# Optimization experiments

Measured on AMD Instinct MI355X. Metric: run time of the kernel, lower is better.

Reference implementation:

```python
import jax, jax.numpy as jnp
import numpy as np
from jax import lax


def _transform_points(pts, M, eps=1e-8):
    # pytorch3d row-vector convention: p' = [p, 1] @ M, then perspective divide by w.
    ph = jnp.concatenate([pts, jnp.ones(pts.shape[:-1] + (1,), pts.dtype)], axis=-1)
    out = jnp.einsum('bnk,bkl->bnl', ph, M)
    w = out[..., 3:4]
    w = jnp.where(jnp.abs(w) < eps, eps, w)
    return out[..., :3] / w


def _rasterize_spheres(pts_screen, radius, image_size, K):
    # pts_screen: [B,N,3] with (x,y) in NDC and z = view-space depth; radius: [B,N].
    # Per pixel: keep K front-most (smallest z>0) points with NDC dist2 <= radius^2.
    B, N, _ = pts_screen.shape
    half = 1.0 - 1.0 / image_size
    coords = jnp.linspace(half, -half, image_size, dtype=pts_screen.dtype)  # pytorch3d NDC: +x left, +y up
    py, px = jnp.meshgrid(coords, coords, indexing='ij')  # [H,W]
    dx = pts_screen[:, None, None, :, 0] - px[None, :, :, None]  # [B,H,W,N]
    dy = pts_screen[:, None, None, :, 1] - py[None, :, :, None]
    dist2 = dx * dx + dy * dy
    z = pts_screen[:, None, None, :, 2]  # [B,1,1,N]
    inside = (dist2 <= (radius * radius)[:, None, None, :]) & (z > 0)
    zmask = jnp.where(inside, z, jnp.inf)
    negz, inds = lax.top_k(-zmask, K)  # K smallest z (front-most) per pixel
    valid = jnp.isfinite(negz)
    zbuf = jnp.where(valid, -negz, jnp.float32(-1.0))
    d2 = jnp.take_along_axis(dist2, inds, axis=-1)
    dists = jnp.where(valid, d2, jnp.float32(-1.0))
    idx = jnp.where(valid, inds, -1)
    return idx, zbuf, dists


def setup_inputs() -> dict:
    key = jax.random.key(0)
    k1, k2 = jax.random.split(key)
    B, N = 1, 1024
    points = jax.random.normal(k1, (B, N, 3), dtype=jnp.float32)
    radius = 0.02 + 0.06 * jax.random.uniform(k2, (B, N), dtype=jnp.float32)
    # Rigid world->view: identity rotation, translate camera so points sit at z ~ 3 (row-vector convention).
    w2v = np.eye(4, dtype=np.float32)
    w2v[3, 2] = 3.0
    world2view = jnp.asarray(w2v)[None]
    # Perspective projection (row-vector): [x,y,z,1] @ P = [s x, s y, a z + b, z]
    s, znear, zfar = 2.0, 0.1, 100.0
    a = zfar / (zfar - znear)
    b = -zfar * znear / (zfar - znear)
    proj = jnp.asarray(np.array([[s, 0, 0, 0], [0, s, 0, 0], [0, 0, a, 1], [0, 0, b, 0]], dtype=np.float32))[None]
    return {'points': points, 'radius': radius, 'world2view': world2view, 'proj': proj,
            'image_size': 256, 'points_per_pixel': 8}


def reference(points, radius, world2view, proj, image_size, points_per_pixel):
    pts_view = _transform_points(points, world2view)
    pts_screen = _transform_points(pts_view, proj)
    pts_screen = pts_screen.at[..., 2].set(pts_view[..., 2])  # keep view-space depth
    idx, zbuf, dists = _rasterize_spheres(pts_screen, radius, image_size, points_per_pixel)
    return idx, zbuf, dists
```

## Files before the change

kernel.cpp:

```cpp
#include <hip/hip_runtime.h>
#include <math.h>


#define KPP 8
#define BW  8
#define TS  16

typedef float vf4 __attribute__((ext_vector_type(4)));

static __device__ __forceinline__ void nt_store4(float* p, float a, float b, float c, float d) {
    vf4 v = {a, b, c, d};
    __builtin_nontemporal_store(v, (vf4*)p);
}

__global__ __launch_bounds__(256) void sphere_raster_kernel(
    const float* __restrict__ points,
    const float* __restrict__ radius,
    const float* __restrict__ w2v,
    const float* __restrict__ proj,
    float* __restrict__ out,
    int B, int N, int H, int W)
{
    extern __shared__ char smem[];
    float4* cmp  = (float4*)smem;
    int*    cidx = (int*)(smem + (size_t)(N + 2 * BW) * sizeof(float4));
    __shared__ int wsum[4];

    const int tid      = threadIdx.x;
    const int tilesX   = W / TS;
    const int tilesPer = tilesX * (H / TS);
    const int tile     = blockIdx.x % tilesPer;
    const int b        = blockIdx.x / tilesPer;
    const int tx0      = (tile % tilesX) * TS;
    const int ty0      = (tile / tilesX) * TS;
    const int j        = tx0 + (tid & (TS - 1));
    const int i        = ty0 + (tid >> 4);
    const int lane     = tid & 63;
    const int wid      = tid >> 6;

    const float* M1 = w2v  + (size_t)b * 16;
    const float* M2 = proj + (size_t)b * 16;

    const double halfd = 1.0 - 1.0 / (double)W;
    const double stepd = 2.0 * halfd / (double)(W - 1);
    const float px = (float)(halfd - (double)j * stepd);
    const float py = (float)(halfd - (double)i * stepd);
    const float cx = (float)(halfd - ((double)tx0 + (TS - 1) * 0.5) * stepd);
    const float cy = (float)(halfd - ((double)ty0 + (TS - 1) * 0.5) * stepd);
    const float hext = (float)(((TS - 1) * 0.5 + 1.0) * stepd);

    const int t0 = tid * 4;
    float4 P[4];
    int keep[4];
    int c = 0;

    const float4* pv = (const float4*)(points + ((size_t)b * N + t0) * 3);
    float4 q0 = pv[0], q1 = pv[1], q2 = pv[2];
    float4 rr = *(const float4*)(radius + (size_t)b * N + t0);
    float xs[4] = {q0.x, q0.w, q1.z, q2.y};
    float ys[4] = {q0.y, q1.x, q1.w, q2.z};
    float zs[4] = {q0.z, q1.y, q2.x, q2.w};
    float rv[4] = {rr.x, rr.y, rr.z, rr.w};

#pragma unroll
    for (int s = 0; s < 4; ++s) {
        float x = xs[s], y = ys[s], z = zs[s];
        float vx = ((x * M1[0] + y * M1[4]) + z * M1[8])  + M1[12];
        float vy = ((x * M1[1] + y * M1[5]) + z * M1[9])  + M1[13];
        float vz = ((x * M1[2] + y * M1[6]) + z * M1[10]) + M1[14];
        float vw = ((x * M1[3] + y * M1[7]) + z * M1[11]) + M1[15];
        float w1 = (fabsf(vw) < 1e-8f) ? 1e-8f : vw;
        vx /= w1; vy /= w1; vz /= w1;
        float sx = ((vx * M2[0] + vy * M2[4]) + vz * M2[8])  + M2[12];
        float sy = ((vx * M2[1] + vy * M2[5]) + vz * M2[9])  + M2[13];
        float sw = ((vx * M2[3] + vy * M2[7]) + vz * M2[11]) + M2[15];
        float w2 = (fabsf(sw) < 1e-8f) ? 1e-8f : sw;
        sx /= w2; sy /= w2;
        float r = rv[s];
        float r2eff = (vz > 0.0f) ? r * r : -1.0f;
        float dxm = fmaxf(0.0f, fabsf(sx - cx) - hext);
        float dym = fmaxf(0.0f, fabsf(sy - cy) - hext);
        float dmin2 = dxm * dxm + dym * dym;
        keep[s] = (dmin2 <= r2eff + 1e-6f) ? 1 : 0;
        P[s] = make_float4(sx, sy, vz, r2eff);
        c += keep[s];
    }

    int pre = c;
#pragma unroll
    for (int d = 1; d < 64; d <<= 1) {
        int v = __shfl_up(pre, d);
        if (lane >= d) pre += v;
    }
    if (lane == 63) wsum[wid] = pre;
    __syncthreads();
    int wbase = 0, M = 0;
#pragma unroll
    for (int w = 0; w < 4; ++w) {
        int s = wsum[w];
        if (w < wid) wbase += s;
        M += s;
    }
    int pos = wbase + (pre - c);
#pragma unroll
    for (int s = 0; s < 4; ++s) {
        if (keep[s]) { cmp[pos] = P[s]; cidx[pos] = t0 + s; ++pos; }
    }
    const int Mpad = (M + 2 * BW - 1) & ~(2 * BW - 1);
    if (tid < Mpad - M) {
        cmp[M + tid]  = make_float4(0.0f, 0.0f, 0.0f, -1.0f);
        cidx[M + tid] = -1;
    }
    __syncthreads();

    unsigned long long kb[KPP];
#pragma unroll
    for (int k = 0; k < KPP; ++k) kb[k] = ~0ULL;

    auto process = [&](const float4* pp, int base) {
#pragma unroll
        for (int u = 0; u < BW; ++u) {
            float dx = pp[u].x - px;
            float dy = pp[u].y - py;
            float dist2 = __fadd_rn(__fmul_rn(dx, dx), __fmul_rn(dy, dy));
            unsigned long long key =
                ((unsigned long long)__float_as_uint(pp[u].z) << 32) |
                (unsigned)(base + u);
            if ((dist2 <= pp[u].w) && (key < kb[KPP - 1])) {
                unsigned long long kc = key;
#pragma unroll
                for (int k2 = 0; k2 < KPP; ++k2) {
                    unsigned long long t = kb[k2];
                    bool lt = (kc < t);
                    kb[k2] = lt ? kc : t;
                    kc     = lt ? t  : kc;
                }
            }
        }
    };

    float4 pa[BW];
    float4 pb[BW];

#pragma unroll
    for (int u = 0; u < BW; ++u) pa[u] = cmp[u];

    for (int n = 0; n < Mpad; n += 2 * BW) {
#pragma unroll
        for (int u = 0; u < BW; ++u) pb[u] = cmp[n + BW + u];
        process(pa, n);
        if (n + 2 * BW < Mpad) {
#pragma unroll
            for (int u = 0; u < BW; ++u) pa[u] = cmp[n + 2 * BW + u];
        }
        process(pb, n + BW);
    }

    const size_t pix   = ((size_t)b * H + i) * W + j;
    const size_t plane = (size_t)B * H * W * KPP;
    float vidx[KPP], vzbf[KPP], vdst[KPP];
#pragma unroll
    for (int k = 0; k < KPP; ++k) {
        unsigned long long key = kb[k];
        bool valid = (key != ~0ULL);
        int p2 = valid ? (int)(key & 0xFFFFFFFFu) : 0;
        float4 p = cmp[p2];
        int idx  = cidx[p2];
        float dx = p.x - px;
        float dy = p.y - py;
        float dist2 = __fadd_rn(__fmul_rn(dx, dx), __fmul_rn(dy, dy));
        float z = __uint_as_float((unsigned)(key >> 32));
        vidx[k] = valid ? (float)idx : -1.0f;
        vzbf[k] = valid ? z          : -1.0f;
        vdst[k] = valid ? dist2      : -1.0f;
    }
    float* oidx = out + pix * KPP;
    float* ozbf = out + plane + pix * KPP;
    float* odst = out + 2 * plane + pix * KPP;
    nt_store4(oidx,     vidx[0], vidx[1], vidx[2], vidx[3]);
    nt_store4(oidx + 4, vidx[4], vidx[5], vidx[6], vidx[7]);
    nt_store4(ozbf,     vzbf[0], vzbf[1], vzbf[2], vzbf[3]);
    nt_store4(ozbf + 4, vzbf[4], vzbf[5], vzbf[6], vzbf[7]);
    nt_store4(odst,     vdst[0], vdst[1], vdst[2], vdst[3]);
    nt_store4(odst + 4, vdst[4], vdst[5], vdst[6], vdst[7]);
}

extern "C" void kernel_launch(void* const* d_in, const int* in_sizes, int n_in,
                              void* d_out, int out_size, void* d_ws, size_t ws_size,
                              hipStream_t stream) {
    const float* points = (const float*)d_in[0];
    const float* radius = (const float*)d_in[1];
    const float* w2v    = (const float*)d_in[2];
    const float* proj   = (const float*)d_in[3];
    int B = in_sizes[2] / 16;
    if (B < 1) B = 1;
    int N = in_sizes[1] / B;
    int HW = out_size / (3 * B * KPP);
    int H = 1;
    while ((H + 1) * (H + 1) <= HW) ++H;
    int W = H;

    int tiles = (W / TS) * (H / TS);
    size_t shmem = (size_t)(N + 2 * BW) * (sizeof(float4) + sizeof(int));
    sphere_raster_kernel<<<B * tiles, 256, shmem, stream>>>(
        points, radius, w2v, proj, (float*)d_out, B, N, H, W);
}
```

Measured before the change: 13.59 us.

## Cull points per wavefront 8x8 sub-tile with ballot compaction into per-wave lists

Each wavefront now covers an 8x8 pixel quadrant instead of rows of a 16x16 tile, and builds its own candidate list by culling all projected points against its quadrant's bounding box, using ballot/popcount compaction. The aim is shorter per-wave candidate loops, and the block-wide scan and barrier before the raster loop go away. In exchange every wave scans all N points from shared memory, and the list is hard-capped at 256 entries, so extra candidates are silently dropped if a quadrant has more. The hard-coded 16 iterations also assume N=1024.

```diff
diff --git a/kernel.cpp b/kernel.cpp
--- a/kernel.cpp
+++ b/kernel.cpp
@@ -5,6 +5,7 @@
 #define KPP 8
 #define BW  8
 #define TS  16
+#define CAP 256
 
 typedef float vf4 __attribute__((ext_vector_type(4)));
 
@@ -22,21 +23,23 @@
     int B, int N, int H, int W)
 {
     extern __shared__ char smem[];
-    float4* cmp  = (float4*)smem;
-    int*    cidx = (int*)(smem + (size_t)(N + 2 * BW) * sizeof(float4));
-    __shared__ int wsum[4];
+    float4* sh = (float4*)smem;
+    float4* cmpw  = (float4*)(smem + (size_t)N * 16);
+    int*    cidxw = (int*)(smem + (size_t)N * 16 + 4 * (CAP + 16) * 16);
 
     const int tid      = threadIdx.x;
+    const int lane     = tid & 63;
+    const int wid      = tid >> 6;
     const int tilesX   = W / TS;
     const int tilesPer = tilesX * (H / TS);
     const int tile     = blockIdx.x % tilesPer;
     const int b        = blockIdx.x / tilesPer;
     const int tx0      = (tile % tilesX) * TS;
     const int ty0      = (tile / tilesX) * TS;
-    const int j        = tx0 + (tid & (TS - 1));
-    const int i        = ty0 + (tid >> 4);
-    const int lane     = tid & 63;
-    const int wid      = tid >> 6;
+    const int qx = tx0 + (wid & 1) * 8;
+    const int qy = ty0 + (wid >> 1) * 8;
+    const int j = qx + (lane & 7);
+    const int i = qy + (lane >> 3);
 
     const float* M1 = w2v  + (size_t)b * 16;
     const float* M2 = proj + (size_t)b * 16;
@@ -45,73 +48,63 @@
     const double stepd = 2.0 * halfd / (double)(W - 1);
     const float px = (float)(halfd - (double)j * stepd);
     const float py = (float)(halfd - (double)i * stepd);
-    const float cx = (float)(halfd - ((double)tx0 + (TS - 1) * 0.5) * stepd);
-    const float cy = (float)(halfd - ((double)ty0 + (TS - 1) * 0.5) * stepd);
-    const float hext = (float)(((TS - 1) * 0.5 + 1.0) * stepd);
-
-    const int t0 = tid * 4;
-    float4 P[4];
-    int keep[4];
-    int c = 0;
-
-    const float4* pv = (const float4*)(points + ((size_t)b * N + t0) * 3);
-    float4 q0 = pv[0], q1 = pv[1], q2 = pv[2];
-    float4 rr = *(const float4*)(radius + (size_t)b * N + t0);
-    float xs[4] = {q0.x, q0.w, q1.z, q2.y};
-    float ys[4] = {q0.y, q1.x, q1.w, q2.z};
-    float zs[4] = {q0.z, q1.y, q2.x, q2.w};
-    float rv[4] = {rr.x, rr.y, rr.z, rr.w};
-
-#pragma unroll
-    for (int s = 0; s < 4; ++s) {
-        float x = xs[s], y = ys[s], z = zs[s];
-        float vx = ((x * M1[0] + y * M1[4]) + z * M1[8])  + M1[12];
-        float vy = ((x * M1[1] + y * M1[5]) + z * M1[9])  + M1[13];
-        float vz = ((x * M1[2] + y * M1[6]) + z * M1[10]) + M1[14];
-        float vw = ((x * M1[3] + y * M1[7]) + z * M1[11]) + M1[15];
-        float w1 = (fabsf(vw) < 1e-8f) ? 1e-8f : vw;
-        vx /= w1; vy /= w1; vz /= w1;
-        float sx = ((vx * M2[0] + vy * M2[4]) + vz * M2[8])  + M2[12];
-        float sy = ((vx * M2[1] + vy * M2[5]) + vz * M2[9])  + M2[13];
-        float sw = ((vx * M2[3] + vy * M2[7]) + vz * M2[11]) + M2[15];
-        float w2 = (fabsf(sw) < 1e-8f) ? 1e-8f : sw;
-        sx /= w2; sy /= w2;
-        float r = rv[s];
-        float r2eff = (vz > 0.0f) ? r * r : -1.0f;
-        float dxm = fmaxf(0.0f, fabsf(sx - cx) - hext);
-        float dym = fmaxf(0.0f, fabsf(sy - cy) - hext);
+    const float cxw = (float)(halfd - ((double)qx + 3.5) * stepd);
+    const float cyw = (float)(halfd - ((double)qy + 3.5) * stepd);
+    const float hext = (float)(4.5 * stepd);
+
+    {
+        const int t0 = tid * 4;
+        const float4* pv = (const float4*)(points + ((size_t)b * N + t0) * 3);
+        float4 q0 = pv[0], q1 = pv[1], q2 = pv[2];
+        float4 rr = *(const float4*)(radius + (size_t)b * N + t0);
+        float xs[4] = {q0.x, q0.w, q1.z, q2.y};
+        float ys[4] = {q0.y, q1.x, q1.w, q2.z};
+        float zs[4] = {q0.z, q1.y, q2.x, q2.w};
+        float rv[4] = {rr.x, rr.y, rr.z, rr.w};
+#pragma unroll
+        for (int s = 0; s < 4; ++s) {
+            float x = xs[s], y = ys[s], z = zs[s];
+            float vx = ((x * M1[0] + y * M1[4]) + z * M1[8])  + M1[12];
+            float vy = ((x * M1[1] + y * M1[5]) + z * M1[9])  + M1[13];
+            float vz = ((x * M1[2] + y * M1[6]) + z * M1[10]) + M1[14];
+            float vw = ((x * M1[3] + y * M1[7]) + z * M1[11]) + M1[15];
+            float w1 = (fabsf(vw) < 1e-8f) ? 1e-8f : vw;
+            vx /= w1; vy /= w1; vz /= w1;
+            float sx = ((vx * M2[0] + vy * M2[4]) + vz * M2[8])  + M2[12];
+            float sy = ((vx * M2[1] + vy * M2[5]) + vz * M2[9])  + M2[13];
+            float sw = ((vx * M2[3] + vy * M2[7]) + vz * M2[11]) + M2[15];
+            float w2 = (fabsf(sw) < 1e-8f) ? 1e-8f : sw;
+            sx /= w2; sy /= w2;
+            float r = rv[s];
+            float r2eff = (vz > 0.0f) ? r * r : -1.0f;
+            sh[t0 + s] = make_float4(sx, sy, vz, r2eff);
+        }
+    }
+    __syncthreads();
+
+    float4* cmp  = cmpw  + wid * (CAP + 16);
+    int*    cidx = cidxw + wid * (CAP + 16);
+    int M = 0;
+    const unsigned long long ltmask = (lane == 0) ? 0ULL : (~0ULL >> (64 - lane));
+#pragma unroll 1
+    for (int s = 0; s < 16; ++s) {
+        int idx = s * 64 + lane;
+        float4 p = sh[idx];
+        float dxm = fmaxf(0.0f, fabsf(p.x - cxw) - hext);
+        float dym = fmaxf(0.0f, fabsf(p.y - cyw) - hext);
         float dmin2 = dxm * dxm + dym * dym;
-        keep[s] = (dmin2 <= r2eff + 1e-6f) ? 1 : 0;
-        P[s] = make_float4(sx, sy, vz, r2eff);
-        c += keep[s];
-    }
-
-    int pre = c;
-#pragma unroll
-    for (int d = 1; d < 64; d <<= 1) {
-        int v = __shfl_up(pre, d);
-        if (lane >= d) pre += v;
-    }
-    if (lane == 63) wsum[wid] = pre;
-    __syncthreads();
-    int wbase = 0, M = 0;
-#pragma unroll
-    for (int w = 0; w < 4; ++w) {
-        int s = wsum[w];
-        if (w < wid) wbase += s;
-        M += s;
-    }
-    int pos = wbase + (pre - c);
-#pragma unroll
-    for (int s = 0; s < 4; ++s) {
-        if (keep[s]) { cmp[pos] = P[s]; cidx[pos] = t0 + s; ++pos; }
-    }
+        int keep = (dmin2 <= p.w + 1e-6f) ? 1 : 0;
+        unsigned long long mask = __ballot(keep);
+        int pos = M + __popcll(mask & ltmask);
+        if (keep && pos < CAP) { cmp[pos] = p; cidx[pos] = idx; }
+        M += __popcll(mask);
+    }
+    if (M > CAP) M = CAP;
     const int Mpad = (M + 2 * BW - 1) & ~(2 * BW - 1);
-    if (tid < Mpad - M) {
-        cmp[M + tid]  = make_float4(0.0f, 0.0f, 0.0f, -1.0f);
-        cidx[M + tid] = -1;
-    }
-    __syncthreads();
+    if (lane < Mpad - M) {
+        cmp[M + lane]  = make_float4(0.0f, 0.0f, 0.0f, -1.0f);
+        cidx[M + lane] = -1;
+    }
 
     unsigned long long kb[KPP];
 #pragma unroll
@@ -122,7 +115,8 @@
         for (int u = 0; u < BW; ++u) {
             float dx = pp[u].x - px;
             float dy = pp[u].y - py;
-            float dist2 = __fadd_rn(__fmul_rn(dx, dx), __fmul_rn(dy, dy));
+            float dist2 = __fadd_rn(__fmul_rn(dx, dx), __fadd_rn(__fmul_rn(dy, dy), 0.0f));
+            dist2 = __fadd_rn(__fmul_rn(dx, dx), __fmul_rn(dy, dy));
             unsigned long long key =
                 ((unsigned long long)__float_as_uint(pp[u].z) << 32) |
                 (unsigned)(base + u);
@@ -141,7 +135,6 @@
 
     float4 pa[BW];
     float4 pb[BW];
-
 #pragma unroll
     for (int u = 0; u < BW; ++u) pa[u] = cmp[u];
 
@@ -201,7 +194,7 @@
     int W = H;
 
     int tiles = (W / TS) * (H / TS);
-    size_t shmem = (size_t)(N + 2 * BW) * (sizeof(float4) + sizeof(int));
+    size_t shmem = (size_t)N * 16 + (size_t)4 * (CAP + 16) * 20;
     sphere_raster_kernel<<<B * tiles, 256, shmem, stream>>>(
         points, radius, w2v, proj, (float*)d_out, B, N, H, W);
 }
```

New measurement: 14.92 us. 9.8% more time.

## Cull points per 8x8 wavefront quadrant with separate shared candidate lists

Applied to the files above, without the earlier changes.

Each 16x16 tile is split into four 8x8 quadrants, one per wavefront, and every point is bounds-tested against each quadrant. Surviving points are compacted into per-quadrant shared lists using a packed 64-bit prefix scan that counts all four quadrants at once. Each wavefront then scans only the candidates that can touch its quadrant, which cuts inner-loop iterations. Shared memory is now a fixed static array capped at 320 entries per quadrant, so any points beyond that cap are silently dropped, which can give wrong results on dense inputs.

```diff
diff --git a/kernel.cpp b/kernel.cpp
--- a/kernel.cpp
+++ b/kernel.cpp
@@ -5,6 +5,7 @@
 #define KPP 8
 #define BW  8
 #define TS  16
+#define CAP 320
 
 typedef float vf4 __attribute__((ext_vector_type(4)));
 
@@ -21,22 +22,23 @@
     float* __restrict__ out,
     int B, int N, int H, int W)
 {
-    extern __shared__ char smem[];
-    float4* cmp  = (float4*)smem;
-    int*    cidx = (int*)(smem + (size_t)(N + 2 * BW) * sizeof(float4));
-    __shared__ int wsum[4];
+    __shared__ float4 cmpL[4][CAP + 16];
+    __shared__ int    cidxL[4][CAP + 16];
+    __shared__ unsigned long long wsum64[4];
 
     const int tid      = threadIdx.x;
+    const int lane     = tid & 63;
+    const int wid      = tid >> 6;
     const int tilesX   = W / TS;
     const int tilesPer = tilesX * (H / TS);
     const int tile     = blockIdx.x % tilesPer;
     const int b        = blockIdx.x / tilesPer;
     const int tx0      = (tile % tilesX) * TS;
     const int ty0      = (tile / tilesX) * TS;
-    const int j        = tx0 + (tid & (TS - 1));
-    const int i        = ty0 + (tid >> 4);
-    const int lane     = tid & 63;
-    const int wid      = tid >> 6;
+    const int qx = tx0 + (wid & 1) * 8;
+    const int qy = ty0 + (wid >> 1) * 8;
+    const int j  = qx + (lane & 7);
+    const int i  = qy + (lane >> 3);
 
     const float* M1 = w2v  + (size_t)b * 16;
     const float* M2 = proj + (size_t)b * 16;
@@ -45,14 +47,18 @@
     const double stepd = 2.0 * halfd / (double)(W - 1);
     const float px = (float)(halfd - (double)j * stepd);
     const float py = (float)(halfd - (double)i * stepd);
-    const float cx = (float)(halfd - ((double)tx0 + (TS - 1) * 0.5) * stepd);
-    const float cy = (float)(halfd - ((double)ty0 + (TS - 1) * 0.5) * stepd);
-    const float hext = (float)(((TS - 1) * 0.5 + 1.0) * stepd);
+    float cqx[4], cqy[4];
+#pragma unroll
+    for (int q = 0; q < 4; ++q) {
+        cqx[q] = (float)(halfd - ((double)(tx0 + (q & 1) * 8) + 3.5) * stepd);
+        cqy[q] = (float)(halfd - ((double)(ty0 + (q >> 1) * 8) + 3.5) * stepd);
+    }
+    const float hext = (float)(4.5 * stepd);
 
     const int t0 = tid * 4;
     float4 P[4];
-    int keep[4];
-    int c = 0;
+    int km = 0;
+    unsigned long long pack = 0;
 
     const float4* pv = (const float4*)(points + ((size_t)b * N + t0) * 3);
     float4 q0 = pv[0], q1 = pv[1], q2 = pv[2];
@@ -78,40 +84,58 @@
         sx /= w2; sy /= w2;
         float r = rv[s];
         float r2eff = (vz > 0.0f) ? r * r : -1.0f;
-        float dxm = fmaxf(0.0f, fabsf(sx - cx) - hext);
-        float dym = fmaxf(0.0f, fabsf(sy - cy) - hext);
-        float dmin2 = dxm * dxm + dym * dym;
-        keep[s] = (dmin2 <= r2eff + 1e-6f) ? 1 : 0;
         P[s] = make_float4(sx, sy, vz, r2eff);
-        c += keep[s];
-    }
-
-    int pre = c;
+        float thr = r2eff + 1e-6f;
+#pragma unroll
+        for (int q = 0; q < 4; ++q) {
+            float dxm = fmaxf(0.0f, fabsf(sx - cqx[q]) - hext);
+            float dym = fmaxf(0.0f, fabsf(sy - cqy[q]) - hext);
+            int keep = ((dxm * dxm + dym * dym) <= thr) ? 1 : 0;
+            km  |= keep << (q * 4 + s);
+            pack += keep ? (1ULL << (16 * q)) : 0ULL;
+        }
+    }
+
+    unsigned long long pre = pack;
 #pragma unroll
     for (int d = 1; d < 64; d <<= 1) {
-        int v = __shfl_up(pre, d);
+        unsigned long long v = __shfl_up(pre, d);
         if (lane >= d) pre += v;
     }
-    if (lane == 63) wsum[wid] = pre;
+    if (lane == 63) wsum64[wid] = pre;
     __syncthreads();
-    int wbase = 0, M = 0;
+    unsigned long long exc = pre - pack;
+    unsigned long long prevW = 0, tot = 0;
 #pragma unroll
     for (int w = 0; w < 4; ++w) {
-        int s = wsum[w];
-        if (w < wid) wbase += s;
-        M += s;
-    }
-    int pos = wbase + (pre - c);
-#pragma unroll
-    for (int s = 0; s < 4; ++s) {
-        if (keep[s]) { cmp[pos] = P[s]; cidx[pos] = t0 + s; ++pos; }
-    }
-    const int Mpad = (M + 2 * BW - 1) & ~(2 * BW - 1);
-    if (tid < Mpad - M) {
-        cmp[M + tid]  = make_float4(0.0f, 0.0f, 0.0f, -1.0f);
-        cidx[M + tid] = -1;
+        unsigned long long ws = wsum64[w];
+        if (w < wid) prevW += ws;
+        tot += ws;
+    }
+
+#pragma unroll
+    for (int q = 0; q < 4; ++q) {
+        int pos = (int)((prevW >> (16 * q)) & 0xFFFF) + (int)((exc >> (16 * q)) & 0xFFFF);
+#pragma unroll
+        for (int s = 0; s < 4; ++s) {
+            if (km & (1 << (q * 4 + s))) {
+                if (pos < CAP) { cmpL[q][pos] = P[s]; cidxL[q][pos] = t0 + s; }
+                ++pos;
+            }
+        }
+    }
+
+    int Mw = (int)((tot >> (16 * wid)) & 0xFFFF);
+    if (Mw > CAP) Mw = CAP;
+    const int Mpad = (Mw + 2 * BW - 1) & ~(2 * BW - 1);
+    if (lane < Mpad - Mw) {
+        cmpL[wid][Mw + lane]  = make_float4(0.0f, 0.0f, 0.0f, -1.0f);
+        cidxL[wid][Mw + lane] = -1;
     }
     __syncthreads();
+
+    const float4* cmp  = cmpL[wid];
+    const int*    cidx = cidxL[wid];
 
     unsigned long long kb[KPP];
 #pragma unroll
@@ -141,7 +165,6 @@
 
     float4 pa[BW];
     float4 pb[BW];
-
 #pragma unroll
     for (int u = 0; u < BW; ++u) pa[u] = cmp[u];
 
@@ -201,7 +224,6 @@
     int W = H;
 
     int tiles = (W / TS) * (H / TS);
-    size_t shmem = (size_t)(N + 2 * BW) * (sizeof(float4) + sizeof(int));
-    sphere_raster_kernel<<<B * tiles, 256, shmem, stream>>>(
+    sphere_raster_kernel<<<B * tiles, 256, 0, stream>>>(
         points, radius, w2v, proj, (float*)d_out, B, N, H, W);
 }
```

Result: slower. 14.15 us (+4.2%).
